# Performance work log

Hardware: AMD Instinct MI355X
Metric: run time of the kernel (lower is better)

The kernel has to match this reference:

```python
import jax, jax.numpy as jnp
import numpy as np

T, B, F = 1024, 32, 2048
H, C = 64, 101


def setup_inputs() -> dict:
    key = jax.random.key(0)
    ks = jax.random.split(key, 7)
    s = 0.02
    return {
        "x": jax.random.normal(ks[0], (T, B, F), dtype=jnp.float32),
        "W_ih": jax.random.normal(ks[1], (4 * H, F), dtype=jnp.float32) * s,
        "W_hh": jax.random.normal(ks[2], (4 * H, H), dtype=jnp.float32) * s,
        "b_ih": jax.random.normal(ks[3], (4 * H,), dtype=jnp.float32) * s,
        "b_hh": jax.random.normal(ks[4], (4 * H,), dtype=jnp.float32) * s,
        "W_lin": jax.random.normal(ks[5], (C, H), dtype=jnp.float32) * s,
        "b_lin": jax.random.normal(ks[6], (C,), dtype=jnp.float32) * s,
    }


def reference(x, W_ih, W_hh, b_ih, b_hh, W_lin, b_lin):
    # Sequential LSTMCell over T timesteps, PyTorch gate order (i, f, g, o).
    # Precompute the input projection for all timesteps in one big GEMM;
    # only the tiny [B,H]x[H,4H] recurrent matmul stays inside the scan.
    x_proj = jnp.einsum('tbf,gf->tbg', x, W_ih) + b_ih + b_hh  # [T, B, 4H]

    h0 = jnp.zeros((B, H), dtype=x.dtype)
    c0 = jnp.zeros((B, H), dtype=x.dtype)

    def step(carry, xp_t):
        h, c = carry
        gates = xp_t + h @ W_hh.T  # [B, 4H]
        i, f, g, o = jnp.split(gates, 4, axis=-1)
        c_new = jax.nn.sigmoid(f) * c + jax.nn.sigmoid(i) * jnp.tanh(g)
        h_new = jax.nn.sigmoid(o) * jnp.tanh(c_new)
        return (h_new, c_new), None

    (h_T, _), _ = jax.lax.scan(step, (h0, c0), x_proj)
    # Original module returns only the final step's linear output.
    return h_T @ W_lin.T + b_lin  # [B, C]
```

## Files before the change

kernel.cpp:

```cpp
#include <hip/hip_runtime.h>
#include <hip/hip_bf16.h>
#include <math.h>

#define T_STEPS 1024
#define B_SZ 32
#define F_SZ 2048
#define H_SZ 64
#define G4 256
#define C_SZ 101

typedef __bf16 bf16x8 __attribute__((ext_vector_type(8)));
typedef unsigned short u16x8 __attribute__((ext_vector_type(8)));
typedef unsigned short u16x4 __attribute__((ext_vector_type(4)));
typedef float f32x4 __attribute__((ext_vector_type(4)));
typedef float f32x2 __attribute__((ext_vector_type(2)));
typedef _Float16 f16x4 __attribute__((ext_vector_type(4)));

__device__ __forceinline__ void split_bf16(float f, unsigned short& h,
                                           unsigned short& l) {
  unsigned u = __builtin_bit_cast(unsigned, f);
  unsigned rh = (u + 0x7FFFu + ((u >> 16) & 1u)) >> 16;
  h = (unsigned short)rh;
  float d = f - __builtin_bit_cast(float, rh << 16);
  unsigned ud = __builtin_bit_cast(unsigned, d);
  l = (unsigned short)((ud + 0x7FFFu + ((ud >> 16) & 1u)) >> 16);
}

__device__ __forceinline__ float dot2(float a, float b, float c) {
  float d;
  asm("v_dot2_f32_f16 %0, %1, %2, %3" : "=v"(d) : "v"(a), "v"(b), "v"(c));
  return d;
}

__device__ __forceinline__ float sigm_f(float x) {
  return __builtin_amdgcn_rcpf(1.f + __expf(-x));
}
__device__ __forceinline__ float tanh_f(float x) {
  return 2.f * __builtin_amdgcn_rcpf(1.f + __expf(-2.f * x)) - 1.f;
}

#define REP8(M) M(0) M(1) M(2) M(3) M(4) M(5) M(6) M(7)

__global__ __launch_bounds__(256) void presplit_w(
    const float* __restrict__ W, unsigned short* __restrict__ hi,
    unsigned short* __restrict__ lo) {
  const int idx = (blockIdx.x * 256 + threadIdx.x) * 4;
  float4 v = *(const float4*)(W + idx);
  unsigned short h0, l0, h1, l1, h2, l2, h3, l3;
  split_bf16(v.x, h0, l0);
  split_bf16(v.y, h1, l1);
  split_bf16(v.z, h2, l2);
  split_bf16(v.w, h3, l3);
  *(u16x4*)(hi + idx) = u16x4{h0, h1, h2, h3};
  *(u16x4*)(lo + idx) = u16x4{l0, l1, l2, l3};
}

__global__ __launch_bounds__(256) void whh_to_f16(
    const float* __restrict__ W, _Float16* __restrict__ o) {
  const int idx = (blockIdx.x * 256 + threadIdx.x) * 4;
  float4 v = *(const float4*)(W + idx);
  f16x4 r = {(_Float16)v.x, (_Float16)v.y, (_Float16)v.z, (_Float16)v.w};
  *(f16x4*)(o + idx) = r;
}

#define BM 128
#define BK 32
#define LDSP 40

__global__ __launch_bounds__(512) void xproj_mfma(
    const float* __restrict__ x, const unsigned short* __restrict__ Whi_g,
    const unsigned short* __restrict__ Wlo_g, const float* __restrict__ b_ih,
    const float* __restrict__ b_hh, float* __restrict__ xproj) {
  __shared__ alignas(16) unsigned short Xhi[BM][LDSP];
  __shared__ alignas(16) unsigned short Xlo[BM][LDSP];
  __shared__ alignas(16) unsigned short Whi[G4][LDSP];
  __shared__ alignas(16) unsigned short Wlo[G4][LDSP];

  const int tid = threadIdx.x;
  const int lane = tid & 63;
  const int wave = tid >> 6;
  const int wm = wave >> 2;
  const int wn = wave & 3;
  const size_t R0 = (size_t)blockIdx.x * BM;

  const int xr = tid >> 2;
  const int xs = (tid & 3) * 8;
  const int wr = tid >> 1;
  const int wsg = (tid & 1) * 16;

  const float* xbase = x + (R0 + xr) * (size_t)F_SZ + xs;
  const unsigned short* whb = Whi_g + (size_t)wr * F_SZ + wsg;
  const unsigned short* wlb = Wlo_g + (size_t)wr * F_SZ + wsg;

  float4 xa = *(const float4*)(xbase + 0);
  float4 xb = *(const float4*)(xbase + 4);
  u16x8 wh0 = *(const u16x8*)(whb + 0);
  u16x8 wh1 = *(const u16x8*)(whb + 8);
  u16x8 wl0 = *(const u16x8*)(wlb + 0);
  u16x8 wl1 = *(const u16x8*)(wlb + 8);

  f32x4 acc[4][4] = {};

  const int ar = lane & 15;
  const int ak = (lane >> 4) * 8;

  for (int kt = 0; kt < F_SZ; kt += BK) {
    {
      float xf[8] = {xa.x, xa.y, xa.z, xa.w, xb.x, xb.y, xb.z, xb.w};
      u16x8 xh, xl;
#pragma unroll
      for (int i = 0; i < 8; ++i) {
        unsigned short h, l;
        split_bf16(xf[i], h, l);
        xh[i] = h;
        xl[i] = l;
      }
      *(u16x8*)&Xhi[xr][xs] = xh;
      *(u16x8*)&Xlo[xr][xs] = xl;
      *(u16x8*)&Whi[wr][wsg] = wh0;
      *(u16x8*)&Whi[wr][wsg + 8] = wh1;
      *(u16x8*)&Wlo[wr][wsg] = wl0;
      *(u16x8*)&Wlo[wr][wsg + 8] = wl1;
    }
    __syncthreads();

    const int ktn = (kt + BK < F_SZ) ? kt + BK : kt;
    xa = *(const float4*)(xbase + ktn + 0);
    xb = *(const float4*)(xbase + ktn + 4);
    wh0 = *(const u16x8*)(whb + ktn + 0);
    wh1 = *(const u16x8*)(whb + ktn + 8);
    wl0 = *(const u16x8*)(wlb + ktn + 0);
    wl1 = *(const u16x8*)(wlb + ktn + 8);

    bf16x8 Ah[4], Al[4], Bh[4], Bl[4];
#pragma unroll
    for (int fm = 0; fm < 4; ++fm) {
      const int row = wm * 64 + fm * 16 + ar;
      Ah[fm] = __builtin_bit_cast(bf16x8, *(const u16x8*)&Xhi[row][ak]);
      Al[fm] = __builtin_bit_cast(bf16x8, *(const u16x8*)&Xlo[row][ak]);
    }
#pragma unroll
    for (int fn = 0; fn < 4; ++fn) {
      const int col = wn * 64 + fn * 16 + ar;
      Bh[fn] = __builtin_bit_cast(bf16x8, *(const u16x8*)&Whi[col][ak]);
      Bl[fn] = __builtin_bit_cast(bf16x8, *(const u16x8*)&Wlo[col][ak]);
    }
#pragma unroll
    for (int fm = 0; fm < 4; ++fm) {
#pragma unroll
      for (int fn = 0; fn < 4; ++fn) {
        acc[fm][fn] = __builtin_amdgcn_mfma_f32_16x16x32_bf16(
            Ah[fm], Bh[fn], acc[fm][fn], 0, 0, 0);
        acc[fm][fn] = __builtin_amdgcn_mfma_f32_16x16x32_bf16(
            Ah[fm], Bl[fn], acc[fm][fn], 0, 0, 0);
        acc[fm][fn] = __builtin_amdgcn_mfma_f32_16x16x32_bf16(
            Al[fm], Bh[fn], acc[fm][fn], 0, 0, 0);
      }
    }
    __syncthreads();
  }

  const int cr = (lane >> 4) * 4;
  const int cc = lane & 15;
#pragma unroll
  for (int fn = 0; fn < 4; ++fn) {
    const int gj = wn * 64 + fn * 16 + cc;
    const float bias = b_ih[gj] + b_hh[gj];
#pragma unroll
    for (int fm = 0; fm < 4; ++fm) {
      const size_t gr = R0 + wm * 64 + fm * 16 + cr;
#pragma unroll
      for (int r = 0; r < 4; ++r) {
        xproj[(gr + r) * G4 + gj] = acc[fm][fn][r] + bias;
      }
    }
  }
}

__global__ __attribute__((amdgpu_flat_work_group_size(64, 64)))
__attribute__((amdgpu_waves_per_eu(1, 1))) void lstm_scan_f16(
    const float* __restrict__ xproj, const _Float16* __restrict__ Whh16,
    float* __restrict__ hT) {
  const int b = blockIdx.x;
  const int u = threadIdx.x;

  __shared__ alignas(16) _Float16 hbuf[2][H_SZ];

  const _Float16* wp = Whh16 + (size_t)u * H_SZ;
#define PINW(i)                                                               \
  f32x4 w0_##i, w1_##i, w2_##i, w3_##i;                                       \
  {                                                                           \
    const _Float16* a0 = wp + 0 * 4096 + 8 * (i);                             \
    const _Float16* a1 = wp + 1 * 4096 + 8 * (i);                             \
    const _Float16* a2 = wp + 2 * 4096 + 8 * (i);                             \
    const _Float16* a3 = wp + 3 * 4096 + 8 * (i);                             \
    asm volatile("global_load_dwordx4 %0, %1, off" : "=v"(w0_##i) : "v"(a0)); \
    asm volatile("global_load_dwordx4 %0, %1, off" : "=v"(w1_##i) : "v"(a1)); \
    asm volatile("global_load_dwordx4 %0, %1, off" : "=v"(w2_##i) : "v"(a2)); \
    asm volatile("global_load_dwordx4 %0, %1, off" : "=v"(w3_##i) : "v"(a3)); \
  }
  REP8(PINW)
#undef PINW
  asm volatile("s_waitcnt vmcnt(0)" ::: "memory");

  hbuf[0][u] = (_Float16)0.f;
  float c = 0.f, hval = 0.f;
  int p = 0;

  const float* a_next = xproj + (size_t)b * G4 + u;
  const size_t step_off = (size_t)B_SZ * G4;

  float xi0, xf0, xg0, xo0, xi1, xf1, xg1, xo1;
  float xi2, xf2, xg2, xo2, xi3, xf3, xg3, xo3;

#define XLOAD(S, a)                                                    \
  asm volatile("global_load_dword %0, %4, off\n\t"                     \
               "global_load_dword %1, %4, off offset:256\n\t"          \
               "global_load_dword %2, %4, off offset:512\n\t"          \
               "global_load_dword %3, %4, off offset:768"              \
               : "=&v"(xi##S), "=&v"(xf##S), "=&v"(xg##S), "=&v"(xo##S) \
               : "v"(a));

  XLOAD(0, a_next) a_next += step_off;
  XLOAD(1, a_next) a_next += step_off;
  XLOAD(2, a_next) a_next += step_off;
  XLOAD(3, a_next) a_next += step_off;

  for (int it = 0; it < T_STEPS / 4; ++it) {
    const int tb = it * 4;

#define SLOT(S)                                                               \
    {                                                                         \
                        \
      asm volatile("s_waitcnt vmcnt(12)"                                      \
                   : "+v"(xi##S), "+v"(xf##S), "+v"(xg##S), "+v"(xo##S));     \
      const f32x4 hq_0 = *(const f32x4*)&hbuf[p][0];                          \
      const f32x4 hq_1 = *(const f32x4*)&hbuf[p][8];                          \
      const f32x4 hq_2 = *(const f32x4*)&hbuf[p][16];                         \
      const f32x4 hq_3 = *(const f32x4*)&hbuf[p][24];                         \
      const f32x4 hq_4 = *(const f32x4*)&hbuf[p][32];                         \
      const f32x4 hq_5 = *(const f32x4*)&hbuf[p][40];                         \
      const f32x4 hq_6 = *(const f32x4*)&hbuf[p][48];                         \
      const f32x4 hq_7 = *(const f32x4*)&hbuf[p][56];                         \
      float aiA = xi##S, aiB = 0.f, afA = xf##S, afB = 0.f;                   \
      float agA = xg##S, agB = 0.f, aoA = xo##S, aoB = 0.f;                   \
      DOTQ(aiA, 0, w0) DOTQ(aiA, 1, w0) DOTQ(aiA, 2, w0) DOTQ(aiA, 3, w0)     \
      DOTQ(aiB, 4, w0) DOTQ(aiB, 5, w0) DOTQ(aiB, 6, w0) DOTQ(aiB, 7, w0)     \
      DOTQ(afA, 0, w1) DOTQ(afA, 1, w1) DOTQ(afA, 2, w1) DOTQ(afA, 3, w1)     \
      DOTQ(afB, 4, w1) DOTQ(afB, 5, w1) DOTQ(afB, 6, w1) DOTQ(afB, 7, w1)     \
      DOTQ(agA, 0, w2) DOTQ(agA, 1, w2) DOTQ(agA, 2, w2) DOTQ(agA, 3, w2)     \
      DOTQ(agB, 4, w2) DOTQ(agB, 5, w2) DOTQ(agB, 6, w2) DOTQ(agB, 7, w2)     \
      DOTQ(aoA, 0, w3) DOTQ(aoA, 1, w3) DOTQ(aoA, 2, w3) DOTQ(aoA, 3, w3)     \
      DOTQ(aoB, 4, w3) DOTQ(aoB, 5, w3) DOTQ(aoB, 6, w3) DOTQ(aoB, 7, w3)     \
      const float pi = aiA + aiB;                                             \
      const float pf = afA + afB;                                             \
      const float pg = agA + agB;                                             \
      const float po = aoA + aoB;                                             \
      c = sigm_f(pf) * c + sigm_f(pi) * tanh_f(pg);                           \
      hval = sigm_f(po) * tanh_f(c);                                          \
      hbuf[p ^ 1][u] = (_Float16)hval;                                        \
      p ^= 1;                                                                 \
         \
      XLOAD(S, a_next)                                                        \
      if (tb + (S) + 4 < T_STEPS - 1) a_next += step_off;                     \
    }

#define DOTQ(acc, i, wg)                         \
    acc = dot2(hq_##i[0], wg##_##i[0], acc);     \
    acc = dot2(hq_##i[1], wg##_##i[1], acc);     \
    acc = dot2(hq_##i[2], wg##_##i[2], acc);     \
    acc = dot2(hq_##i[3], wg##_##i[3], acc);

    SLOT(0)
    SLOT(1)
    SLOT(2)
    SLOT(3)

#undef DOTQ
#undef SLOT
  }
#undef XLOAD

  hT[b * H_SZ + u] = hval;
}

__global__ __launch_bounds__(128) void final_linear_kernel(
    const float* __restrict__ hT, const float* __restrict__ W_lin,
    const float* __restrict__ b_lin, float* __restrict__ out) {
  const int b = blockIdx.x;
  const int cc = threadIdx.x;

  __shared__ float h_l[H_SZ];
  if (threadIdx.x < H_SZ) h_l[threadIdx.x] = hT[b * H_SZ + threadIdx.x];
  __syncthreads();

  if (cc < C_SZ) {
    float acc = b_lin[cc];
    const float* wr = W_lin + (size_t)cc * H_SZ;
#pragma unroll
    for (int k = 0; k < H_SZ; ++k) acc += h_l[k] * wr[k];
    out[b * C_SZ + cc] = acc;
  }
}

extern "C" void kernel_launch(void* const* d_in, const int* in_sizes, int n_in,
                              void* d_out, int out_size, void* d_ws,
                              size_t ws_size, hipStream_t stream) {
  const float* x = (const float*)d_in[0];
  const float* W_ih = (const float*)d_in[1];
  const float* W_hh = (const float*)d_in[2];
  const float* b_ih = (const float*)d_in[3];
  const float* b_hh = (const float*)d_in[4];
  const float* W_lin = (const float*)d_in[5];
  const float* b_lin = (const float*)d_in[6];
  float* out = (float*)d_out;

  const size_t XP_BYTES = (size_t)T_STEPS * B_SZ * G4 * sizeof(float);
  float* xproj = (float*)d_ws;
  float* hT = (float*)((char*)d_ws + XP_BYTES);
  unsigned short* Whi_g = (unsigned short*)((char*)d_ws + XP_BYTES + 8192);
  unsigned short* Wlo_g = Whi_g + (size_t)G4 * F_SZ;
  _Float16* Whh16 = (_Float16*)(Wlo_g + (size_t)G4 * F_SZ);

  presplit_w<<<512, 256, 0, stream>>>(W_ih, Whi_g, Wlo_g);
  whh_to_f16<<<16, 256, 0, stream>>>(W_hh, Whh16);
  xproj_mfma<<<(T_STEPS * B_SZ) / BM, 512, 0, stream>>>(x, Whi_g, Wlo_g, b_ih,
                                                        b_hh, xproj);
  lstm_scan_f16<<<B_SZ, 64, 0, stream>>>(xproj, Whh16, hT);
  final_linear_kernel<<<B_SZ, 128, 0, stream>>>(hT, W_lin, b_lin, out);
}
```

Measured before the change: 553.0 us.

## Compute recurrent h·W_hh matvec with MFMA tiles instead of dot2 chains

Replaces each thread's 64 v_dot2 instructions per step with 32 MFMA 16x16x32 f16 ops per wavefront. The h vector is broadcast as the A operand and W_hh is pinned in registers as B tiles, then each lane picks its gate value out of the accumulator with selects. The aim is to shorten the latency of the serial per-step dependency chain. In exchange, most MFMA output is wasted because only one row is useful, and MFMA issue latency now sits on the critical path.

Result: faster. 536.9 us (-2.9%).

```diff
diff --git a/kernel.cpp b/kernel.cpp
--- a/kernel.cpp
+++ b/kernel.cpp
@@ -13,8 +13,8 @@
 typedef unsigned short u16x8 __attribute__((ext_vector_type(8)));
 typedef unsigned short u16x4 __attribute__((ext_vector_type(4)));
 typedef float f32x4 __attribute__((ext_vector_type(4)));
-typedef float f32x2 __attribute__((ext_vector_type(2)));
 typedef _Float16 f16x4 __attribute__((ext_vector_type(4)));
+typedef _Float16 f16x8 __attribute__((ext_vector_type(8)));
 
 __device__ __forceinline__ void split_bf16(float f, unsigned short& h,
                                            unsigned short& l) {
@@ -26,12 +26,6 @@
   l = (unsigned short)((ud + 0x7FFFu + ((ud >> 16) & 1u)) >> 16);
 }
 
-__device__ __forceinline__ float dot2(float a, float b, float c) {
-  float d;
-  asm("v_dot2_f32_f16 %0, %1, %2, %3" : "=v"(d) : "v"(a), "v"(b), "v"(c));
-  return d;
-}
-
 __device__ __forceinline__ float sigm_f(float x) {
   return __builtin_amdgcn_rcpf(1.f + __expf(-x));
 }
@@ -39,7 +33,16 @@
   return 2.f * __builtin_amdgcn_rcpf(1.f + __expf(-2.f * x)) - 1.f;
 }
 
+__device__ __forceinline__ float sel4(float a0, float a1, float a2, float a3,
+                                      bool k1, bool k2) {
+  const float t0 = k1 ? a1 : a0;
+  const float t1 = k1 ? a3 : a2;
+  return k2 ? t1 : t0;
+}
+
 #define REP8(M) M(0) M(1) M(2) M(3) M(4) M(5) M(6) M(7)
+#define REP16(M) M(0) M(1) M(2) M(3) M(4) M(5) M(6) M(7) \
+                 M(8) M(9) M(10) M(11) M(12) M(13) M(14) M(15)
 
 __global__ __launch_bounds__(256) void presplit_w(
     const float* __restrict__ W, unsigned short* __restrict__ hi,
@@ -178,46 +181,45 @@
 }
 
 __global__ __attribute__((amdgpu_flat_work_group_size(64, 64)))
-__attribute__((amdgpu_waves_per_eu(1, 1))) void lstm_scan_f16(
+__attribute__((amdgpu_waves_per_eu(1, 1))) void lstm_scan_mfma(
     const float* __restrict__ xproj, const _Float16* __restrict__ Whh16,
     float* __restrict__ hT) {
   const int b = blockIdx.x;
-  const int u = threadIdx.x;
+  const int l = threadIdx.x;
+  const int kg8 = (l >> 4) * 8;
+  const bool k1 = ((l >> 4) & 1) != 0;
+  const bool k2 = ((l >> 4) & 2) != 0;
 
   __shared__ alignas(16) _Float16 hbuf[2][H_SZ];
 
-  const _Float16* wp = Whh16 + (size_t)u * H_SZ;
-#define PINW(i)                                                               \
-  f32x4 w0_##i, w1_##i, w2_##i, w3_##i;                                       \
+  const _Float16* wb = Whh16 + (size_t)(l & 15) * H_SZ + kg8;
+#define PINB(n)                                                               \
+  f32x4 wB0_##n, wB1_##n;                                                     \
   {                                                                           \
-    const _Float16* a0 = wp + 0 * 4096 + 8 * (i);                             \
-    const _Float16* a1 = wp + 1 * 4096 + 8 * (i);                             \
-    const _Float16* a2 = wp + 2 * 4096 + 8 * (i);                             \
-    const _Float16* a3 = wp + 3 * 4096 + 8 * (i);                             \
-    asm volatile("global_load_dwordx4 %0, %1, off" : "=v"(w0_##i) : "v"(a0)); \
-    asm volatile("global_load_dwordx4 %0, %1, off" : "=v"(w1_##i) : "v"(a1)); \
-    asm volatile("global_load_dwordx4 %0, %1, off" : "=v"(w2_##i) : "v"(a2)); \
-    asm volatile("global_load_dwordx4 %0, %1, off" : "=v"(w3_##i) : "v"(a3)); \
-  }
-  REP8(PINW)
-#undef PINW
+    const _Float16* a0_##n = wb + (n) * (16 * H_SZ);                          \
+    const _Float16* a1_##n = wb + (n) * (16 * H_SZ) + 32;                     \
+    asm volatile("global_load_dwordx4 %0, %1, off" : "=v"(wB0_##n) : "v"(a0_##n)); \
+    asm volatile("global_load_dwordx4 %0, %1, off" : "=v"(wB1_##n) : "v"(a1_##n)); \
+  }
+  REP16(PINB)
+#undef PINB
   asm volatile("s_waitcnt vmcnt(0)" ::: "memory");
 
-  hbuf[0][u] = (_Float16)0.f;
+  hbuf[0][l] = (_Float16)0.f;
   float c = 0.f, hval = 0.f;
   int p = 0;
 
-  const float* a_next = xproj + (size_t)b * G4 + u;
+  const float* a_next = xproj + (size_t)b * G4 + l;
   const size_t step_off = (size_t)B_SZ * G4;
 
   float xi0, xf0, xg0, xo0, xi1, xf1, xg1, xo1;
   float xi2, xf2, xg2, xo2, xi3, xf3, xg3, xo3;
 
-#define XLOAD(S, a)                                                    \
-  asm volatile("global_load_dword %0, %4, off\n\t"                     \
-               "global_load_dword %1, %4, off offset:256\n\t"          \
-               "global_load_dword %2, %4, off offset:512\n\t"          \
-               "global_load_dword %3, %4, off offset:768"              \
+#define XLOAD(S, a)                                                     \
+  asm volatile("global_load_dword %0, %4, off\n\t"                      \
+               "global_load_dword %1, %4, off offset:256\n\t"           \
+               "global_load_dword %2, %4, off offset:512\n\t"           \
+               "global_load_dword %3, %4, off offset:768"               \
                : "=&v"(xi##S), "=&v"(xf##S), "=&v"(xg##S), "=&v"(xo##S) \
                : "v"(a));
 
@@ -229,59 +231,51 @@
   for (int it = 0; it < T_STEPS / 4; ++it) {
     const int tb = it * 4;
 
+#define TILE(n)                                                               \
+    f32x4 acc_##n = {0.f, 0.f, 0.f, 0.f};                                     \
+    acc_##n = __builtin_amdgcn_mfma_f32_16x16x32_f16(                         \
+        hA0, __builtin_bit_cast(f16x8, wB0_##n), acc_##n, 0, 0, 0);           \
+    acc_##n = __builtin_amdgcn_mfma_f32_16x16x32_f16(                         \
+        hA1, __builtin_bit_cast(f16x8, wB1_##n), acc_##n, 0, 0, 0);
+
 #define SLOT(S)                                                               \
     {                                                                         \
-                        \
+                              \
       asm volatile("s_waitcnt vmcnt(12)"                                      \
                    : "+v"(xi##S), "+v"(xf##S), "+v"(xg##S), "+v"(xo##S));     \
-      const f32x4 hq_0 = *(const f32x4*)&hbuf[p][0];                          \
-      const f32x4 hq_1 = *(const f32x4*)&hbuf[p][8];                          \
-      const f32x4 hq_2 = *(const f32x4*)&hbuf[p][16];                         \
-      const f32x4 hq_3 = *(const f32x4*)&hbuf[p][24];                         \
-      const f32x4 hq_4 = *(const f32x4*)&hbuf[p][32];                         \
-      const f32x4 hq_5 = *(const f32x4*)&hbuf[p][40];                         \
-      const f32x4 hq_6 = *(const f32x4*)&hbuf[p][48];                         \
-      const f32x4 hq_7 = *(const f32x4*)&hbuf[p][56];                         \
-      float aiA = xi##S, aiB = 0.f, afA = xf##S, afB = 0.f;                   \
-      float agA = xg##S, agB = 0.f, aoA = xo##S, aoB = 0.f;                   \
-      DOTQ(aiA, 0, w0) DOTQ(aiA, 1, w0) DOTQ(aiA, 2, w0) DOTQ(aiA, 3, w0)     \
-      DOTQ(aiB, 4, w0) DOTQ(aiB, 5, w0) DOTQ(aiB, 6, w0) DOTQ(aiB, 7, w0)     \
-      DOTQ(afA, 0, w1) DOTQ(afA, 1, w1) DOTQ(afA, 2, w1) DOTQ(afA, 3, w1)     \
-      DOTQ(afB, 4, w1) DOTQ(afB, 5, w1) DOTQ(afB, 6, w1) DOTQ(afB, 7, w1)     \
-      DOTQ(agA, 0, w2) DOTQ(agA, 1, w2) DOTQ(agA, 2, w2) DOTQ(agA, 3, w2)     \
-      DOTQ(agB, 4, w2) DOTQ(agB, 5, w2) DOTQ(agB, 6, w2) DOTQ(agB, 7, w2)     \
-      DOTQ(aoA, 0, w3) DOTQ(aoA, 1, w3) DOTQ(aoA, 2, w3) DOTQ(aoA, 3, w3)     \
-      DOTQ(aoB, 4, w3) DOTQ(aoB, 5, w3) DOTQ(aoB, 6, w3) DOTQ(aoB, 7, w3)     \
-      const float pi = aiA + aiB;                                             \
-      const float pf = afA + afB;                                             \
-      const float pg = agA + agB;                                             \
-      const float po = aoA + aoB;                                             \
+        \
+      const f16x8 hA0 = *(const f16x8*)&hbuf[p][kg8];                         \
+      const f16x8 hA1 = *(const f16x8*)&hbuf[p][32 + kg8];                    \
+      REP16(TILE)                                                             \
+             \
+      const float di = sel4(acc_0[0], acc_1[0], acc_2[0], acc_3[0], k1, k2);  \
+      const float df = sel4(acc_4[0], acc_5[0], acc_6[0], acc_7[0], k1, k2);  \
+      const float dg = sel4(acc_8[0], acc_9[0], acc_10[0], acc_11[0], k1, k2);\
+      const float dq = sel4(acc_12[0], acc_13[0], acc_14[0], acc_15[0], k1, k2);\
+      const float pi = xi##S + di;                                            \
+      const float pf = xf##S + df;                                            \
+      const float pg = xg##S + dg;                                            \
+      const float po = xo##S + dq;                                            \
       c = sigm_f(pf) * c + sigm_f(pi) * tanh_f(pg);                           \
       hval = sigm_f(po) * tanh_f(c);                                          \
-      hbuf[p ^ 1][u] = (_Float16)hval;                                        \
+      hbuf[p ^ 1][l] = (_Float16)hval;                                        \
       p ^= 1;                                                                 \
          \
       XLOAD(S, a_next)                                                        \
       if (tb + (S) + 4 < T_STEPS - 1) a_next += step_off;                     \
     }
 
-#define DOTQ(acc, i, wg)                         \
-    acc = dot2(hq_##i[0], wg##_##i[0], acc);     \
-    acc = dot2(hq_##i[1], wg##_##i[1], acc);     \
-    acc = dot2(hq_##i[2], wg##_##i[2], acc);     \
-    acc = dot2(hq_##i[3], wg##_##i[3], acc);
-
     SLOT(0)
     SLOT(1)
     SLOT(2)
     SLOT(3)
 
-#undef DOTQ
 #undef SLOT
+#undef TILE
   }
 #undef XLOAD
 
-  hT[b * H_SZ + u] = hval;
+  hT[b * H_SZ + l] = hval;
 }
 
 __global__ __launch_bounds__(128) void final_linear_kernel(
@@ -326,6 +320,6 @@
   whh_to_f16<<<16, 256, 0, stream>>>(W_hh, Whh16);
   xproj_mfma<<<(T_STEPS * B_SZ) / BM, 512, 0, stream>>>(x, Whi_g, Wlo_g, b_ih,
                                                         b_hh, xproj);
-  lstm_scan_f16<<<B_SZ, 64, 0, stream>>>(xproj, Whh16, hT);
+  lstm_scan_mfma<<<B_SZ, 64, 0, stream>>>(xproj, Whh16, hT);
   final_linear_kernel<<<B_SZ, 128, 0, stream>>>(hT, W_lin, b_lin, out);
 }
```
